# Kernel tuning notes

Measured on AMD Instinct MI355X. Metric: run time of the kernel, lower is better.

## Reference

```python
import jax, jax.numpy as jnp
import numpy as np

B = 16
H_DIM = 512
N_HEADS = 8
HEAD_DIM = H_DIM // N_HEADS  # 64
EPS = 1e-5
DST_LENS = 256 + 16 * np.arange(B)  # ragged dst sizes, total 6016
SRC_LENS = 512 - 8 * np.arange(B)   # ragged src sizes, total 7232


def _pad_info(lens):
    # gather/scatter indices to move between flat ragged layout and [B, Lmax, D]
    lens = np.asarray(lens)
    off = np.concatenate([[0], np.cumsum(lens)[:-1]])
    gid = np.repeat(np.arange(len(lens)), lens)
    pos = np.arange(int(lens.sum())) - np.repeat(off, lens)
    Lmax = int(lens.max())
    mask = jnp.asarray(np.arange(Lmax)[None, :] < lens[:, None])
    return gid, pos, Lmax, mask


def _bn(x, g, b):
    # BatchNorm1d forward with batch statistics (training-mode normalization)
    m = x.mean(0)
    v = ((x - m) ** 2).mean(0)
    return (x - m) / jnp.sqrt(v + EPS) * g + b


def setup_inputs() -> dict:
    key = jax.random.key(0)
    ks = jax.random.split(key, 20)
    total_src = int(SRC_LENS.sum())
    total_dst = int(DST_LENS.sum())
    w = lambda k, shape: jax.random.normal(k, shape, jnp.float32) * 0.02
    return {
        "src_h": jax.random.normal(ks[0], (total_src, H_DIM), jnp.float32),
        "dst_h": jax.random.normal(ks[1], (total_dst, H_DIM), jnp.float32),
        "src_num_verts": jnp.asarray(SRC_LENS, jnp.int32),
        "dst_num_verts": jnp.asarray(DST_LENS, jnp.int32),
        "Wq": w(ks[2], (H_DIM, H_DIM)), "bq": w(ks[3], (H_DIM,)),
        "Wk": w(ks[4], (H_DIM, H_DIM)), "bk": w(ks[5], (H_DIM,)),
        "Wv": w(ks[6], (H_DIM, H_DIM)), "bv": w(ks[7], (H_DIM,)),
        "Wm": w(ks[8], (H_DIM, H_DIM)), "bm": w(ks[9], (H_DIM,)),
        "W1": w(ks[10], (H_DIM, 2 * H_DIM)), "b1": w(ks[11], (H_DIM,)),
        "g1": jnp.ones((H_DIM,), jnp.float32), "be1": jnp.zeros((H_DIM,), jnp.float32),
        "W2": w(ks[12], (H_DIM, H_DIM)), "b2": w(ks[13], (H_DIM,)),
        "g2": jnp.ones((H_DIM,), jnp.float32), "be2": jnp.zeros((H_DIM,), jnp.float32),
    }


def reference(src_h, dst_h, src_num_verts, dst_num_verts,
              Wq, bq, Wk, bk, Wv, bv, Wm, bm,
              W1, b1, g1, be1, W2, b2, g2, be2):
    s_lens = np.asarray(src_num_verts)
    d_lens = np.asarray(dst_num_verts)
    sg, sp, Ls, smask = _pad_info(s_lens)
    dg, dp, Ld, dmask = _pad_info(d_lens)

    # ragged -> padded [B, L, D]
    src_pad = jnp.zeros((B, Ls, H_DIM), src_h.dtype).at[sg, sp].set(src_h)
    dst_pad = jnp.zeros((B, Ld, H_DIM), dst_h.dtype).at[dg, dp].set(dst_h)

    # Conv1d(k=1) projections; channel c = d*num_heads + h -> reshape (head_dim, n_heads)
    q = (dst_pad @ Wq.T + bq).reshape(B, Ld, HEAD_DIM, N_HEADS)
    k = (src_pad @ Wk.T + bk).reshape(B, Ls, HEAD_DIM, N_HEADS)
    v = (src_pad @ Wv.T + bv).reshape(B, Ls, HEAD_DIM, N_HEADS)

    scores = jnp.einsum('bndh,bmdh->bhnm', q, k) / 8.0  # sqrt(head_dim)=8
    scores = jnp.where(smask[:, None, None, :], scores, -1e9)
    attn = jax.nn.softmax(scores, axis=-1)
    o = jnp.einsum('bhnm,bmdh->bndh', attn, v).reshape(B, Ld, H_DIM)
    o = o @ Wm.T + bm  # merge Conv1d(k=1)

    # padded -> ragged
    h_msg = o[dg, dp]  # [total_dst, h_dim]

    h = dst_h
    x = jnp.concatenate([h, h_msg], axis=-1)
    x = _bn(x @ W1.T + b1, g1, be1)
    x = jax.nn.relu(x)
    x = _bn(x @ W2.T + b2, g2, be2)
    return h + x
```

## Files before the change

### kernel.cpp

```cpp
#include <hip/hip_runtime.h>
#include <hip/hip_bf16.h>

#define H_DIM 512
#define N_HEADS 8
#define HEAD_DIM 64
#define NBATCH 16

typedef __attribute__((ext_vector_type(8))) short short8;
typedef __attribute__((ext_vector_type(4))) float floatx4;

typedef unsigned short us16;

#define SW3(r) ((((r) >> 1) & 3) | (((r) & 1) << 2))

#define PERMC(c) ((((c) & 7) << 6) | ((c) >> 3))
#define IPERMC(cp) ((((cp) & 63) << 3) | ((cp) >> 6))

__device__ inline unsigned short f2bf(float f) {
  unsigned int u = __float_as_uint(f);
  unsigned int r = (u + 0x7fffu + ((u >> 16) & 1u)) >> 16;
  return (unsigned short)r;
}

__device__ inline void gld16(const us16* g, us16* l) {
  __builtin_amdgcn_global_load_lds(
      (const __attribute__((address_space(1))) void*)g,
      (__attribute__((address_space(3))) void*)l, 16, 0, 0);
}

__global__ __launch_bounds__(256) void prep_all(
    const float* __restrict__ src_h, const float* __restrict__ dst_h,
    const float* __restrict__ Wq, const float* __restrict__ Wk,
    const float* __restrict__ Wv, const float* __restrict__ W1,
    const float* __restrict__ W2, const float* __restrict__ Wm,
    const float* __restrict__ b1, const float* __restrict__ bm,
    us16* __restrict__ src_bf, us16* __restrict__ dst_bf,
    us16* __restrict__ Wqb, us16* __restrict__ Wkv, us16* __restrict__ Wf,
    us16* __restrict__ W2b, float* __restrict__ b1p, float* __restrict__ st,
    int n_src, int n_dst) {
  __shared__ __align__(16) us16 As[64 * 48];
  __shared__ __align__(16) us16 Bs[64 * 48];
  const int blk = blockIdx.x;
  const int t = threadIdx.x;

  if (blk < 2048) {
    if (blk == 0) {
      float4 z = make_float4(0.f, 0.f, 0.f, 0.f);
      ((float4*)st)[t] = z;
      ((float4*)st)[t + 256] = z;
    }
    const float* srcs[7] = {src_h, dst_h, Wq, Wk, Wv, W1, W2};
    us16* dsts[7] = {src_bf, dst_bf, Wqb, Wkv, Wkv + 262144, Wf, W2b};
    int ns[7] = {n_src, n_dst, 262144, 262144, 262144, 262144, 262144};
    const int md_[7] = {0, 0, 2, 2, 0, 1, 0};
    for (int rg = 0; rg < 7; ++rg) {
      const float* sp = srcs[rg];
      us16* dp = dsts[rg];
      const int mode = md_[rg];
      for (int i = (blk * 256 + t) * 4; i < ns[rg]; i += 2048 * 256 * 4) {
        int js, jd;
        if (mode == 1) {
          js = ((i >> 9) * 1024) + (i & 511);
          jd = js;
        } else if (mode == 2) {
          int r = i >> 9;
          js = i;
          jd = (PERMC(r) << 9) + (i & 511);
        } else {
          js = i; jd = i;
        }
        float4 v = *(const float4*)(sp + js);
        ushort4 o;
        o.x = f2bf(v.x); o.y = f2bf(v.y); o.z = f2bf(v.z); o.w = f2bf(v.w);
        *(ushort4*)(dp + jd) = o;
      }
    }
  } else if (blk < 2112) {
    const int bx = (blk - 2048) & 7, byk = (blk - 2048) >> 3;
    const int w = t >> 6, lane = t & 63;
    const int lane15 = lane & 15, quad = lane >> 4;
    const int wm = w >> 1, wn = w & 1;
    const int bn_ = bx * 64, bk = byk * 64;
    floatx4 acc[2][2];
#pragma unroll
    for (int a = 0; a < 2; ++a)
#pragma unroll
      for (int c = 0; c < 2; ++c) acc[a][c] = (floatx4){0.f, 0.f, 0.f, 0.f};
    for (int j0 = 0; j0 < 512; j0 += 32) {
      {
        int n = t >> 2, jj0 = (t & 3) * 8;
        const float* rp = W1 + (size_t)(bn_ + n) * 1024 + 512 + j0 + jj0;
        float4 va = *(const float4*)(rp);
        float4 vb = *(const float4*)(rp + 4);
        ushort4 pa, pb;
        pa.x = f2bf(va.x); pa.y = f2bf(va.y); pa.z = f2bf(va.z); pa.w = f2bf(va.w);
        pb.x = f2bf(vb.x); pb.y = f2bf(vb.y); pb.z = f2bf(vb.z); pb.w = f2bf(vb.w);
        *(ushort4*)(As + n * 48 + jj0) = pa;
        *(ushort4*)(As + n * 48 + jj0 + 4) = pb;
      }
      {
        int jj = t >> 3, kc0 = (t & 7) * 8;
        const float* rp = Wm + (size_t)(j0 + jj) * 512 + bk + kc0;
        float4 va = *(const float4*)(rp);
        float4 vb = *(const float4*)(rp + 4);
        float vv[8] = {va.x, va.y, va.z, va.w, vb.x, vb.y, vb.z, vb.w};
#pragma unroll
        for (int e = 0; e < 8; ++e) Bs[(kc0 + e) * 48 + jj] = f2bf(vv[e]);
      }
      __syncthreads();
      short8 a_[2], b_[2];
#pragma unroll
      for (int mt = 0; mt < 2; ++mt)
        a_[mt] = *(const short8*)(As + (wm * 32 + mt * 16 + lane15) * 48 + quad * 8);
#pragma unroll
      for (int nt = 0; nt < 2; ++nt)
        b_[nt] = *(const short8*)(Bs + (wn * 32 + nt * 16 + lane15) * 48 + quad * 8);
#pragma unroll
      for (int mt = 0; mt < 2; ++mt)
#pragma unroll
        for (int nt = 0; nt < 2; ++nt)
          acc[mt][nt] = __builtin_amdgcn_mfma_f32_16x16x32_bf16(
              a_[mt], b_[nt], acc[mt][nt], 0, 0, 0);
      __syncthreads();
    }
#pragma unroll
    for (int mt = 0; mt < 2; ++mt) {
      int n0 = bn_ + wm * 32 + mt * 16 + quad * 4;
#pragma unroll
      for (int nt = 0; nt < 2; ++nt) {
        int k = bk + wn * 32 + nt * 16 + lane15;
        int kp = PERMC(k);
#pragma unroll
        for (int r = 0; r < 4; ++r)
          Wf[(size_t)(n0 + r) * 1024 + 512 + kp] = f2bf(acc[mt][nt][r]);
      }
    }
  } else {
    int n = (blk - 2112) * 256 + t;
    if (n < 512) {
      const float* rp = W1 + (size_t)n * 1024 + 512;
      float s = 0.f;
      for (int j = 0; j < 512; j += 4) {
        float4 a = *(const float4*)(rp + j);
        float4 c = *(const float4*)(bm + j);
        s += a.x * c.x + a.y * c.y + a.z * c.z + a.w * c.w;
      }
      b1p[n] = b1[n] + s;
    }
  }
}

__device__ inline void gemm_body(
    const us16* __restrict__ A1, const us16* __restrict__ A2,
    const us16* __restrict__ W,
    const float* __restrict__ bias0, const float* __restrict__ bias1,
    void* __restrict__ C0, void* __restrict__ C1, float* __restrict__ stats,
    int M, int N, int K, int mode, int bx, int by) {
  __shared__ __align__(16) us16 As[2 * 64 * 64];
  __shared__ __align__(16) us16 Bs[2 * 128 * 64];
  const int t = threadIdx.x, w = t >> 6, lane = t & 63;
  const int lane15 = lane & 15, quad = lane >> 4;
  const int bm = bx * 64, bn = by * 128;
  const int lrow = lane >> 3;
  const int sl = lane & 7;

  floatx4 acc[4][2];
#pragma unroll
  for (int a = 0; a < 4; ++a)
#pragma unroll
    for (int c = 0; c < 2; ++c) acc[a][c] = (floatx4){0.f, 0.f, 0.f, 0.f};

  const int nk = K >> 6;

#define ISSUE(i, b)                                                          \
  {                                                                          \
    int k0 = (i) << 6;                                                       \
    const us16* Ab = (k0 < 512) ? A1 : A2;                                   \
    int ka = k0 & 511;                                                       \
    _Pragma("unroll")                                                        \
    for (int p = 0; p < 2; ++p) {                                            \
      int rbase = p * 32 + w * 8;                                            \
      int row = rbase + lrow;                                                \
      int kg = sl ^ SW3(row);                                                \
      gld16(Ab + (size_t)(bm + row) * 512 + ka + kg * 8,                     \
            As + (b) * 4096 + rbase * 64);                                   \
    }                                                                        \
    _Pragma("unroll")                                                        \
    for (int p = 0; p < 4; ++p) {                                            \
      int rbase = p * 32 + w * 8;                                            \
      int row = rbase + lrow;                                                \
      int kg = sl ^ SW3(row);                                                \
      gld16(W + (size_t)(bn + row) * K + k0 + kg * 8,                        \
            Bs + (b) * 8192 + rbase * 64);                                   \
    }                                                                        \
  }

  ISSUE(0, 0);
  if (nk > 1) ISSUE(1, 1);
  for (int i = 0; i < nk; ++i) {
    const int cur = i & 1;
    if (i + 1 < nk) {
      asm volatile("s_waitcnt vmcnt(6)" ::: "memory");
    } else {
      asm volatile("s_waitcnt vmcnt(0)" ::: "memory");
    }
    __builtin_amdgcn_s_barrier();
    asm volatile("" ::: "memory");
#pragma unroll
    for (int kh = 0; kh < 2; ++kh) {
      const int g = kh * 4 + quad;
      short8 a_[4], b_[2];
#pragma unroll
      for (int mt = 0; mt < 4; ++mt) {
        int r = mt * 16 + lane15;
        a_[mt] = *(const short8*)(As + cur * 4096 + r * 64 + (g ^ SW3(r)) * 8);
      }
#pragma unroll
      for (int nt = 0; nt < 2; ++nt) {
        int c = w * 32 + nt * 16 + lane15;
        b_[nt] = *(const short8*)(Bs + cur * 8192 + c * 64 + (g ^ SW3(c)) * 8);
      }
#pragma unroll
      for (int mt = 0; mt < 4; ++mt)
#pragma unroll
        for (int nt = 0; nt < 2; ++nt)
          acc[mt][nt] = __builtin_amdgcn_mfma_f32_16x16x32_bf16(
              a_[mt], b_[nt], acc[mt][nt], 0, 0, 0);
    }
    asm volatile("" ::: "memory");
    __builtin_amdgcn_s_barrier();
    asm volatile("" ::: "memory");
    if (i + 2 < nk) ISSUE(i + 2, cur);
  }
#undef ISSUE

  if (mode == 0) {
#pragma unroll
    for (int nt = 0; nt < 2; ++nt) {
      int col = bn + w * 32 + nt * 16 + lane15;
      float bv = bias0[col];
      float s = 0.f, qq = 0.f;
#pragma unroll
      for (int mt = 0; mt < 4; ++mt) {
        int row0 = bm + mt * 16 + quad * 4;
#pragma unroll
        for (int r = 0; r < 4; ++r) {
          float val = acc[mt][nt][r] + bv;
          ((float*)C0)[(size_t)(row0 + r) * N + col] = val;
          s += val; qq = fmaf(val, val, qq);
        }
      }
      s += __shfl_xor(s, 16); s += __shfl_xor(s, 32);
      qq += __shfl_xor(qq, 16); qq += __shfl_xor(qq, 32);
      if (quad == 0) {
        atomicAdd(&stats[col], s);
        atomicAdd(&stats[512 + col], qq);
      }
    }
  } else if (mode == 1) {
#pragma unroll
    for (int nt = 0; nt < 2; ++nt) {
      int col = bn + w * 32 + nt * 16 + lane15;
      float bv = bias0[IPERMC(col)];
#pragma unroll
      for (int mt = 0; mt < 4; ++mt) {
        int row0 = bm + mt * 16 + quad * 4;
#pragma unroll
        for (int r = 0; r < 4; ++r)
          ((us16*)C0)[(size_t)(row0 + r) * 512 + col] = f2bf(acc[mt][nt][r] + bv);
      }
    }
  } else {
#pragma unroll
    for (int nt = 0; nt < 2; ++nt) {
      int col = bn + w * 32 + nt * 16 + lane15;
      if (col < 512) {
        float bv = bias0[IPERMC(col)];
#pragma unroll
        for (int mt = 0; mt < 4; ++mt) {
          int row0 = bm + mt * 16 + quad * 4;
#pragma unroll
          for (int r = 0; r < 4; ++r)
            ((us16*)C0)[(size_t)(row0 + r) * 512 + col] = f2bf(acc[mt][nt][r] + bv);
        }
      } else {
        int cv = col - 512;
        float bv = bias1[cv];
        int plane = (cv & 7) * 64 + (cv >> 3);
#pragma unroll
        for (int mt = 0; mt < 4; ++mt) {
          int row0 = bm + mt * 16 + quad * 4;
          ushort4 pk;
          pk.x = f2bf(acc[mt][nt][0] + bv);
          pk.y = f2bf(acc[mt][nt][1] + bv);
          pk.z = f2bf(acc[mt][nt][2] + bv);
          pk.w = f2bf(acc[mt][nt][3] + bv);
          *(ushort4*)((us16*)C1 + (size_t)plane * M + row0) = pk;
        }
      }
    }
  }
}

__global__ __launch_bounds__(256) void gemm_ffn(
    const us16* __restrict__ A1, const us16* __restrict__ A2,
    const us16* __restrict__ W,
    const float* __restrict__ bias0, void* __restrict__ C0,
    float* __restrict__ stats, int M, int K) {
  int b = blockIdx.x;
  int i = (b & 7) * ((int)gridDim.x >> 3) + (b >> 3);
  gemm_body(A1, A2, W, bias0, nullptr, C0, nullptr, stats, M, 512, K, 0,
            i >> 2, i & 3);
}

__global__ __launch_bounds__(256) void gemm_qkv(
    const us16* __restrict__ dst_bf, const us16* __restrict__ src_bf,
    const us16* __restrict__ Wqb, const us16* __restrict__ Wkv,
    const float* __restrict__ bq, const float* __restrict__ bk,
    const float* __restrict__ bv,
    us16* __restrict__ Qh, us16* __restrict__ Kh, us16* __restrict__ Vt,
    int Md, int Ms) {
  int b = blockIdx.x;
  int i = (b & 7) * ((int)gridDim.x >> 3) + (b >> 3);
  int nq = (Md / 64) * 4;
  if (i < nq) {
    gemm_body(dst_bf, dst_bf, Wqb, bq, nullptr, Qh, nullptr, nullptr,
              Md, 512, 512, 1, i >> 2, i & 3);
  } else {
    int j = i - nq;
    gemm_body(src_bf, src_bf, Wkv, bk, bv, Kh, Vt, nullptr,
              Ms, 1024, 512, 4, j >> 3, j & 7);
  }
}

__global__ __launch_bounds__(256) void gemm_ffn2bn(
    const float* __restrict__ X1, const us16* __restrict__ W,
    const float* __restrict__ st1, const float* __restrict__ g1,
    const float* __restrict__ be1, const float* __restrict__ b2,
    float* __restrict__ X2, float* __restrict__ st2, int M, float invM) {
  __shared__ __align__(16) us16 As[2 * 64 * 64];
  __shared__ __align__(16) us16 Bs[2 * 128 * 64];
  __shared__ float slt[512], tlt[512];
  int b = blockIdx.x;
  int i0 = (b & 7) * ((int)gridDim.x >> 3) + (b >> 3);
  const int bx = i0 >> 2, by = i0 & 3;
  const int t = threadIdx.x, w = t >> 6, lane = t & 63;
  const int lane15 = lane & 15, quad = lane >> 4;
  const int bm = bx * 64, bn = by * 128;
  const int lrow = lane >> 3;
  const int sl = lane & 7;

  for (int c = t; c < 512; c += 256) {
    float mean = st1[c] * invM;
    float var = fmaf(-mean, mean, st1[512 + c] * invM);
    float inv = rsqrtf(var + 1e-5f) * g1[c];
    slt[c] = inv;
    tlt[c] = be1[c] - mean * inv;
  }
  __syncthreads();

  floatx4 acc[4][2];
#pragma unroll
  for (int a = 0; a < 4; ++a)
#pragma unroll
    for (int c = 0; c < 2; ++c) acc[a][c] = (floatx4){0.f, 0.f, 0.f, 0.f};

  const int arow = t >> 2;
  const int ac4 = (t & 3) * 16;
  const int s0 = (t & 3) * 2;

#define ALOAD(dst, ii)                                                       \
  {                                                                          \
    const float* p_ = X1 + (size_t)(bm + arow) * 512 + ((ii) << 6) + ac4;    \
    dst[0] = *(const float4*)(p_);                                           \
    dst[1] = *(const float4*)(p_ + 4);                                       \
    dst[2] = *(const float4*)(p_ + 8);                                       \
    dst[3] = *(const float4*)(p_ + 12);                                      \
  }

#define BISSUE(ii, bb)                                                       \
  {                                                                          \
    int k0 = (ii) << 6;                                                      \
    _Pragma("unroll")                                                        \
    for (int p = 0; p < 4; ++p) {                                            \
      int rbase = p * 32 + w * 8;                                            \
      int row = rbase + lrow;                                                \
      int kg = sl ^ SW3(row);                                                \
      gld16(W + (size_t)(bn + row) * 512 + k0 + kg * 8,                      \
            Bs + (bb) * 8192 + rbase * 64);                                  \
    }                                                                        \
  }

  float4 areg[2][4];
  ALOAD(areg[0], 0);
  BISSUE(0, 0);
  asm volatile("" ::: "memory");
  ALOAD(areg[1], 1);
  BISSUE(1, 1);

#pragma unroll
  for (int i = 0; i < 8; ++i) {
    const int cur = i & 1;
    if (i + 1 < 8) {
      asm volatile("s_waitcnt vmcnt(8)" ::: "memory");
    } else {
      asm volatile("s_waitcnt vmcnt(0)" ::: "memory");
    }
    {
      const int k0 = i << 6;
      __align__(16) us16 vv[16];
#pragma unroll
      for (int q = 0; q < 4; ++q) {
#pragma unroll
        for (int j = 0; j < 4; ++j) {
          int c = k0 + ac4 + q * 4 + j;
          float x = ((const float*)&areg[cur][q])[j];
          float y = fmaxf(fmaf(x, slt[c], tlt[c]), 0.f);
          vv[q * 4 + j] = f2bf(y);
        }
      }
      us16* base = As + cur * 4096 + arow * 64;
      *(short8*)(base + ((s0 ^ SW3(arow)) * 8)) = *(short8*)&vv[0];
      *(short8*)(base + (((s0 + 1) ^ SW3(arow)) * 8)) = *(short8*)&vv[8];
    }
    asm volatile("s_waitcnt lgkmcnt(0)" ::: "memory");
    __builtin_amdgcn_s_barrier();
    asm volatile("" ::: "memory");
#pragma unroll
    for (int kh = 0; kh < 2; ++kh) {
      const int g = kh * 4 + quad;
      short8 a_[4], b_[2];
#pragma unroll
      for (int mt = 0; mt < 4; ++mt) {
        int r = mt * 16 + lane15;
        a_[mt] = *(const short8*)(As + cur * 4096 + r * 64 + (g ^ SW3(r)) * 8);
      }
#pragma unroll
      for (int nt = 0; nt < 2; ++nt) {
        int c = w * 32 + nt * 16 + lane15;
        b_[nt] = *(const short8*)(Bs + cur * 8192 + c * 64 + (g ^ SW3(c)) * 8);
      }
#pragma unroll
      for (int mt = 0; mt < 4; ++mt)
#pragma unroll
        for (int nt = 0; nt < 2; ++nt)
          acc[mt][nt] = __builtin_amdgcn_mfma_f32_16x16x32_bf16(
              a_[mt], b_[nt], acc[mt][nt], 0, 0, 0);
    }
    asm volatile("" ::: "memory");
    __builtin_amdgcn_s_barrier();
    asm volatile("" ::: "memory");
    if (i + 2 < 8) {
      ALOAD(areg[cur], i + 2);
      BISSUE(i + 2, cur);
    }
  }
#undef ALOAD
#undef BISSUE

#pragma unroll
  for (int nt = 0; nt < 2; ++nt) {
    int col = bn + w * 32 + nt * 16 + lane15;
    float bv = b2[col];
    float s = 0.f, qq = 0.f;
#pragma unroll
    for (int mt = 0; mt < 4; ++mt) {
      int row0 = bm + mt * 16 + quad * 4;
#pragma unroll
      for (int r = 0; r < 4; ++r) {
        float val = acc[mt][nt][r] + bv;
        X2[(size_t)(row0 + r) * 512 + col] = val;
        s += val; qq = fmaf(val, val, qq);
      }
    }
    s += __shfl_xor(s, 16); s += __shfl_xor(s, 32);
    qq += __shfl_xor(qq, 16); qq += __shfl_xor(qq, 32);
    if (quad == 0) {
      atomicAdd(&st2[col], s);
      atomicAdd(&st2[512 + col], qq);
    }
  }
}

__global__ __launch_bounds__(256) void attn_v6(
    const us16* __restrict__ Qh, const us16* __restrict__ Kh,
    const us16* __restrict__ Vt, const int* __restrict__ dlens,
    const int* __restrict__ slens, us16* __restrict__ O,
    int Md, int Ms) {
  const int b = blockIdx.x, h = blockIdx.y, tile = blockIdx.z;
  int doff = 0, soff = 0;
  for (int i = 0; i < NBATCH; ++i)
    if (i < b) { doff += dlens[i]; soff += slens[i]; }
  const int dlen = dlens[b], slen = slens[b];
  if (tile * 64 >= dlen) return;

  __shared__ __align__(16) us16 Ks[2 * 64 * 64];
  __shared__ __align__(16) us16 Vts[2 * 64 * 64];
  __shared__ __align__(16) us16 Pw[4][16 * 72];

  const int t = threadIdx.x, wv = t >> 6, lane = t & 63;
  const int lane15 = lane & 15, quad = lane >> 4;
  const int i0w = tile * 64 + wv * 16;
  const bool active = i0w < dlen;

  const us16* Qp = Qh + ((size_t)(doff + (active ? i0w : 0))) * 512 + h * 64;
  const us16* Kp = Kh + ((size_t)soff) * 512 + h * 64;
  const us16* Vtp = Vt + ((size_t)h * 64) * Ms + soff;

  short8 af0 = *(const short8*)(Qp + (size_t)lane15 * 512 + quad * 8);
  short8 af1 = *(const short8*)(Qp + (size_t)lane15 * 512 + 32 + quad * 8);

  floatx4 oa[4];
#pragma unroll
  for (int nt = 0; nt < 4; ++nt) oa[nt] = (floatx4){0.f, 0.f, 0.f, 0.f};
  float m_r[4] = {-3.0e38f, -3.0e38f, -3.0e38f, -3.0e38f};
  float l_r[4] = {0.f, 0.f, 0.f, 0.f};

  const int nc = (slen + 63) >> 6;

#define KVST(c, bu)                                                       \
  {                                                                       \
    int jb = (c) << 6;                                                    \
    _Pragma("unroll")                                                     \
    for (int p = 0; p < 2; ++p) {                                         \
      int row = wv * 16 + p * 8 + (lane >> 3);                            \
      int slt = lane & 7;                                                 \
      int kg = slt ^ SW3(row);                                            \
      gld16(Kp + (size_t)(jb + row) * 512 + kg * 8,                       \
            Ks + (bu) * 4096 + (wv * 16 + p * 8) * 64);                   \
      gld16(Vtp + (size_t)row * Ms + jb + kg * 8,                         \
            Vts + (bu) * 4096 + (wv * 16 + p * 8) * 64);                  \
    }                                                                     \
  }

  KVST(0, 0);
  if (nc > 1) KVST(1, 1);
  for (int c = 0; c < nc; ++c) {
    const int cur = c & 1;
    if (c + 1 < nc) {
      asm volatile("s_waitcnt vmcnt(4)" ::: "memory");
    } else {
      asm volatile("s_waitcnt vmcnt(0)" ::: "memory");
    }
    __builtin_amdgcn_s_barrier();
    asm volatile("" ::: "memory");

    if (active) {
      const int j0 = c << 6;
      floatx4 s[4];
#pragma unroll
      for (int jt = 0; jt < 4; ++jt) {
        int j = jt * 16 + lane15;
        short8 b0 = *(const short8*)(Ks + cur * 4096 + j * 64 + ((quad ^ SW3(j)) * 8));
        short8 b1 = *(const short8*)(Ks + cur * 4096 + j * 64 + (((4 + quad) ^ SW3(j)) * 8));
        floatx4 a = (floatx4){0.f, 0.f, 0.f, 0.f};
        a = __builtin_amdgcn_mfma_f32_16x16x32_bf16(af0, b0, a, 0, 0, 0);
        a = __builtin_amdgcn_mfma_f32_16x16x32_bf16(af1, b1, a, 0, 0, 0);
        s[jt] = a;
      }
      float mx[4] = {-3.0e38f, -3.0e38f, -3.0e38f, -3.0e38f};
#pragma unroll
      for (int jt = 0; jt < 4; ++jt) {
        bool valid = (j0 + jt * 16 + lane15) < slen;
#pragma unroll
        for (int r = 0; r < 4; ++r) {
          float v = valid ? s[jt][r] * 0.125f : -3.0e38f;
          s[jt][r] = v;
          mx[r] = fmaxf(mx[r], v);
        }
      }
#pragma unroll
      for (int r = 0; r < 4; ++r) {
        mx[r] = fmaxf(mx[r], __shfl_xor(mx[r], 1));
        mx[r] = fmaxf(mx[r], __shfl_xor(mx[r], 2));
        mx[r] = fmaxf(mx[r], __shfl_xor(mx[r], 4));
        mx[r] = fmaxf(mx[r], __shfl_xor(mx[r], 8));
      }
      float al[4], sum[4];
#pragma unroll
      for (int r = 0; r < 4; ++r) {
        float mn = fmaxf(m_r[r], mx[r]);
        al[r] = __expf(m_r[r] - mn);
        m_r[r] = mn;
        sum[r] = 0.f;
      }
#pragma unroll
      for (int jt = 0; jt < 4; ++jt)
#pragma unroll
        for (int r = 0; r < 4; ++r) {
          float e = __expf(s[jt][r] - m_r[r]);
          sum[r] += e;
          Pw[wv][(quad * 4 + r) * 72 + jt * 16 + lane15] = f2bf(e);
        }
#pragma unroll
      for (int r = 0; r < 4; ++r) {
        sum[r] += __shfl_xor(sum[r], 1);
        sum[r] += __shfl_xor(sum[r], 2);
        sum[r] += __shfl_xor(sum[r], 4);
        sum[r] += __shfl_xor(sum[r], 8);
        l_r[r] = l_r[r] * al[r] + sum[r];
      }
#pragma unroll
      for (int nt = 0; nt < 4; ++nt)
#pragma unroll
        for (int r = 0; r < 4; ++r) oa[nt][r] *= al[r];
      short8 pa0 = *(const short8*)(&Pw[wv][lane15 * 72 + quad * 8]);
      short8 pa1 = *(const short8*)(&Pw[wv][lane15 * 72 + 32 + quad * 8]);
#pragma unroll
      for (int nt = 0; nt < 4; ++nt) {
        int d = nt * 16 + lane15;
        short8 v0 = *(const short8*)(Vts + cur * 4096 + d * 64 + ((quad ^ SW3(d)) * 8));
        short8 v1 = *(const short8*)(Vts + cur * 4096 + d * 64 + (((4 + quad) ^ SW3(d)) * 8));
        oa[nt] = __builtin_amdgcn_mfma_f32_16x16x32_bf16(pa0, v0, oa[nt], 0, 0, 0);
        oa[nt] = __builtin_amdgcn_mfma_f32_16x16x32_bf16(pa1, v1, oa[nt], 0, 0, 0);
      }
    }

    asm volatile("" ::: "memory");
    __builtin_amdgcn_s_barrier();
    asm volatile("" ::: "memory");
    if (c + 2 < nc) KVST(c + 2, cur);
  }
#undef KVST

  if (active) {
    float linv[4];
#pragma unroll
    for (int r = 0; r < 4; ++r) linv[r] = 1.f / l_r[r];
#pragma unroll
    for (int r = 0; r < 4; ++r) {
      int i = quad * 4 + r;
      us16* orow = O + (size_t)(doff + i0w + i) * H_DIM + h * 64;
#pragma unroll
      for (int nt = 0; nt < 4; ++nt) {
        int d = nt * 16 + lane15;
        orow[d] = f2bf(oa[nt][r] * linv[r]);
      }
    }
  }
}

__global__ __launch_bounds__(256) void bn2_apply(
    const float* __restrict__ X, const float* __restrict__ stats,
    const float* __restrict__ g, const float* __restrict__ be,
    const float* __restrict__ resid, float* __restrict__ Y,
    int M, float invM) {
  const size_t total4 = (size_t)M * (H_DIM / 4);
  for (size_t i = (size_t)blockIdx.x * 256 + threadIdx.x; i < total4;
       i += (size_t)gridDim.x * 256) {
    int c = (int)((i * 4) & (H_DIM - 1));
    float4 x = ((const float4*)X)[i];
    float4 rr = ((const float4*)resid)[i];
    float4 o;
#pragma unroll
    for (int j = 0; j < 4; ++j) {
      int cc = c + j;
      float mean = stats[cc] * invM;
      float var = fmaf(-mean, mean, stats[H_DIM + cc] * invM);
      float inv = rsqrtf(var + 1e-5f) * g[cc];
      float xv = ((const float*)&x)[j];
      ((float*)&o)[j] = (xv - mean) * inv + be[cc] + ((const float*)&rr)[j];
    }
    ((float4*)Y)[i] = o;
  }
}

extern "C" void kernel_launch(void* const* d_in, const int* in_sizes, int n_in,
                              void* d_out, int out_size, void* d_ws, size_t ws_size,
                              hipStream_t stream) {
  const float* src_h = (const float*)d_in[0];
  const float* dst_h = (const float*)d_in[1];
  const int* s_lens  = (const int*)d_in[2];
  const int* d_lens  = (const int*)d_in[3];
  const float* Wq = (const float*)d_in[4];  const float* bq = (const float*)d_in[5];
  const float* Wk = (const float*)d_in[6];  const float* bk = (const float*)d_in[7];
  const float* Wv = (const float*)d_in[8];  const float* bv = (const float*)d_in[9];
  const float* Wm = (const float*)d_in[10]; const float* bm = (const float*)d_in[11];
  const float* W1 = (const float*)d_in[12]; const float* b1 = (const float*)d_in[13];
  const float* g1 = (const float*)d_in[14]; const float* be1 = (const float*)d_in[15];
  const float* W2 = (const float*)d_in[16]; const float* b2 = (const float*)d_in[17];
  const float* g2 = (const float*)d_in[18]; const float* be2 = (const float*)d_in[19];

  const int total_src = in_sizes[0] / H_DIM;
  const int total_dst = in_sizes[1] / H_DIM;

  char* ws = (char*)d_ws;
  us16* src_bf = (us16*)(ws + 0);
  us16* dst_bf = (us16*)(ws + 7405568);
  us16* wbf    = (us16*)(ws + 13565952);
  float* b1p   = (float*)(ws + 16711680);
  us16* Qh     = (us16*)(ws + 17235968);
  us16* Kh     = (us16*)(ws + 23396352);
  us16* Vt     = (us16*)(ws + 30801920);
  us16* Ob     = (us16*)(ws + 38207488);
  float* st    = (float*)(ws + 50528256);
  float* X1    = (float*)(ws + 17235968);
  float* X2    = (float*)(ws + 30801920);
  float* st1 = st, *st2 = st + 1024;

  us16* Wqb = wbf;
  us16* Wkv = wbf + 262144;
  us16* Wf  = wbf + 786432;
  us16* W2b = wbf + 1310720;

  const int mbd = total_dst / 64;
  const int mbs = total_src / 64;
  const dim3 blk256(256);
  const float invM = 1.f / (float)total_dst;

  prep_all<<<dim3(2114), blk256, 0, stream>>>(
      src_h, dst_h, Wq, Wk, Wv, W1, W2, Wm, b1, bm,
      src_bf, dst_bf, Wqb, Wkv, Wf, W2b, b1p, st,
      total_src * H_DIM, total_dst * H_DIM);

  gemm_qkv<<<dim3(mbd * 4 + mbs * 8), blk256, 0, stream>>>(
      dst_bf, src_bf, Wqb, Wkv, bq, bk, bv, Qh, Kh, Vt, total_dst, total_src);

  attn_v6<<<dim3(NBATCH, N_HEADS, 8), blk256, 0, stream>>>(
      Qh, Kh, Vt, d_lens, s_lens, Ob, total_dst, total_src);

  gemm_ffn<<<dim3(mbd * 4), blk256, 0, stream>>>(
      dst_bf, Ob, Wf, b1p, X1, st1, total_dst, 1024);

  gemm_ffn2bn<<<dim3(mbd * 4), blk256, 0, stream>>>(
      X1, W2b, st1, g1, be1, b2, X2, st2, total_dst, invM);

  bn2_apply<<<dim3(512), blk256, 0, stream>>>(
      X2, st2, g2, be2, dst_h, (float*)d_out, total_dst, invM);
}
```

Measured before the change: 220.0 us.

## Fuse fp32-to-bf16 activation conversion into QKV and FFN1 GEMM loaders

Stops pre-converting src_h and dst_h to bf16 in a separate prep pass. The QKV and FFN1 GEMMs now load fp32 activations into registers, convert them, and write swizzled bf16 tiles to LDS, while Ob still streams in through direct global-to-LDS loads. Weight prep (Wf fold, W1/W2 casts, b1p) moves into extra blocks of the QKV launch, and only the Wq/Wk/Wv casts stay in a small prep kernel. This removes a full write and reread of the activations, but the A-operand loads go through registers and VALU conversion, which may hurt the GEMM pipelines. The bn2_apply grid size also changes.

```diff
diff --git a/kernel.cpp b/kernel.cpp
--- a/kernel.cpp
+++ b/kernel.cpp
@@ -28,141 +28,37 @@
       (__attribute__((address_space(3))) void*)l, 16, 0, 0);
 }
 
-__global__ __launch_bounds__(256) void prep_all(
-    const float* __restrict__ src_h, const float* __restrict__ dst_h,
+__global__ __launch_bounds__(256) void prep0(
     const float* __restrict__ Wq, const float* __restrict__ Wk,
-    const float* __restrict__ Wv, const float* __restrict__ W1,
-    const float* __restrict__ W2, const float* __restrict__ Wm,
-    const float* __restrict__ b1, const float* __restrict__ bm,
-    us16* __restrict__ src_bf, us16* __restrict__ dst_bf,
-    us16* __restrict__ Wqb, us16* __restrict__ Wkv, us16* __restrict__ Wf,
-    us16* __restrict__ W2b, float* __restrict__ b1p, float* __restrict__ st,
-    int n_src, int n_dst) {
-  __shared__ __align__(16) us16 As[64 * 48];
-  __shared__ __align__(16) us16 Bs[64 * 48];
-  const int blk = blockIdx.x;
-  const int t = threadIdx.x;
-
-  if (blk < 2048) {
-    if (blk == 0) {
-      float4 z = make_float4(0.f, 0.f, 0.f, 0.f);
-      ((float4*)st)[t] = z;
-      ((float4*)st)[t + 256] = z;
-    }
-    const float* srcs[7] = {src_h, dst_h, Wq, Wk, Wv, W1, W2};
-    us16* dsts[7] = {src_bf, dst_bf, Wqb, Wkv, Wkv + 262144, Wf, W2b};
-    int ns[7] = {n_src, n_dst, 262144, 262144, 262144, 262144, 262144};
-    const int md_[7] = {0, 0, 2, 2, 0, 1, 0};
-    for (int rg = 0; rg < 7; ++rg) {
-      const float* sp = srcs[rg];
-      us16* dp = dsts[rg];
-      const int mode = md_[rg];
-      for (int i = (blk * 256 + t) * 4; i < ns[rg]; i += 2048 * 256 * 4) {
-        int js, jd;
-        if (mode == 1) {
-          js = ((i >> 9) * 1024) + (i & 511);
-          jd = js;
-        } else if (mode == 2) {
-          int r = i >> 9;
-          js = i;
-          jd = (PERMC(r) << 9) + (i & 511);
-        } else {
-          js = i; jd = i;
-        }
-        float4 v = *(const float4*)(sp + js);
-        ushort4 o;
-        o.x = f2bf(v.x); o.y = f2bf(v.y); o.z = f2bf(v.z); o.w = f2bf(v.w);
-        *(ushort4*)(dp + jd) = o;
-      }
-    }
-  } else if (blk < 2112) {
-    const int bx = (blk - 2048) & 7, byk = (blk - 2048) >> 3;
-    const int w = t >> 6, lane = t & 63;
-    const int lane15 = lane & 15, quad = lane >> 4;
-    const int wm = w >> 1, wn = w & 1;
-    const int bn_ = bx * 64, bk = byk * 64;
-    floatx4 acc[2][2];
-#pragma unroll
-    for (int a = 0; a < 2; ++a)
-#pragma unroll
-      for (int c = 0; c < 2; ++c) acc[a][c] = (floatx4){0.f, 0.f, 0.f, 0.f};
-    for (int j0 = 0; j0 < 512; j0 += 32) {
-      {
-        int n = t >> 2, jj0 = (t & 3) * 8;
-        const float* rp = W1 + (size_t)(bn_ + n) * 1024 + 512 + j0 + jj0;
-        float4 va = *(const float4*)(rp);
-        float4 vb = *(const float4*)(rp + 4);
-        ushort4 pa, pb;
-        pa.x = f2bf(va.x); pa.y = f2bf(va.y); pa.z = f2bf(va.z); pa.w = f2bf(va.w);
-        pb.x = f2bf(vb.x); pb.y = f2bf(vb.y); pb.z = f2bf(vb.z); pb.w = f2bf(vb.w);
-        *(ushort4*)(As + n * 48 + jj0) = pa;
-        *(ushort4*)(As + n * 48 + jj0 + 4) = pb;
-      }
-      {
-        int jj = t >> 3, kc0 = (t & 7) * 8;
-        const float* rp = Wm + (size_t)(j0 + jj) * 512 + bk + kc0;
-        float4 va = *(const float4*)(rp);
-        float4 vb = *(const float4*)(rp + 4);
-        float vv[8] = {va.x, va.y, va.z, va.w, vb.x, vb.y, vb.z, vb.w};
-#pragma unroll
-        for (int e = 0; e < 8; ++e) Bs[(kc0 + e) * 48 + jj] = f2bf(vv[e]);
-      }
-      __syncthreads();
-      short8 a_[2], b_[2];
-#pragma unroll
-      for (int mt = 0; mt < 2; ++mt)
-        a_[mt] = *(const short8*)(As + (wm * 32 + mt * 16 + lane15) * 48 + quad * 8);
-#pragma unroll
-      for (int nt = 0; nt < 2; ++nt)
-        b_[nt] = *(const short8*)(Bs + (wn * 32 + nt * 16 + lane15) * 48 + quad * 8);
-#pragma unroll
-      for (int mt = 0; mt < 2; ++mt)
-#pragma unroll
-        for (int nt = 0; nt < 2; ++nt)
-          acc[mt][nt] = __builtin_amdgcn_mfma_f32_16x16x32_bf16(
-              a_[mt], b_[nt], acc[mt][nt], 0, 0, 0);
-      __syncthreads();
-    }
-#pragma unroll
-    for (int mt = 0; mt < 2; ++mt) {
-      int n0 = bn_ + wm * 32 + mt * 16 + quad * 4;
-#pragma unroll
-      for (int nt = 0; nt < 2; ++nt) {
-        int k = bk + wn * 32 + nt * 16 + lane15;
-        int kp = PERMC(k);
-#pragma unroll
-        for (int r = 0; r < 4; ++r)
-          Wf[(size_t)(n0 + r) * 1024 + 512 + kp] = f2bf(acc[mt][nt][r]);
-      }
-    }
-  } else {
-    int n = (blk - 2112) * 256 + t;
-    if (n < 512) {
-      const float* rp = W1 + (size_t)n * 1024 + 512;
-      float s = 0.f;
-      for (int j = 0; j < 512; j += 4) {
-        float4 a = *(const float4*)(rp + j);
-        float4 c = *(const float4*)(bm + j);
-        s += a.x * c.x + a.y * c.y + a.z * c.z + a.w * c.w;
-      }
-      b1p[n] = b1[n] + s;
-    }
-  }
-}
-
-__device__ inline void gemm_body(
-    const us16* __restrict__ A1, const us16* __restrict__ A2,
-    const us16* __restrict__ W,
+    const float* __restrict__ Wv,
+    us16* __restrict__ Wqb, us16* __restrict__ Wkv, float* __restrict__ st) {
+  const int blk = blockIdx.x, t = threadIdx.x;
+  if (blk == 0) {
+    float4 z = make_float4(0.f, 0.f, 0.f, 0.f);
+    ((float4*)st)[t] = z;
+    ((float4*)st)[t + 256] = z;
+  }
+  const int rg = blk >> 8;
+  const float* sp = (rg == 0) ? Wq : (rg == 1) ? Wk : Wv;
+  us16* dp = (rg == 0) ? Wqb : (rg == 1) ? Wkv : (Wkv + 262144);
+  const int i = (((blk & 255) << 8) + t) << 2;
+  float4 v = *(const float4*)(sp + i);
+  ushort4 o;
+  o.x = f2bf(v.x); o.y = f2bf(v.y); o.z = f2bf(v.z); o.w = f2bf(v.w);
+  int jd = (rg < 2) ? ((PERMC(i >> 9) << 9) + (i & 511)) : i;
+  *(ushort4*)(dp + jd) = o;
+}
+
+__device__ inline void qkv_body(
+    const float* __restrict__ actF, const us16* __restrict__ W,
     const float* __restrict__ bias0, const float* __restrict__ bias1,
-    void* __restrict__ C0, void* __restrict__ C1, float* __restrict__ stats,
-    int M, int N, int K, int mode, int bx, int by) {
-  __shared__ __align__(16) us16 As[2 * 64 * 64];
-  __shared__ __align__(16) us16 Bs[2 * 128 * 64];
+    void* __restrict__ C0, void* __restrict__ C1,
+    int M, int mode, int bx, int by, us16* As, us16* Bs) {
   const int t = threadIdx.x, w = t >> 6, lane = t & 63;
   const int lane15 = lane & 15, quad = lane >> 4;
   const int bm = bx * 64, bn = by * 128;
-  const int lrow = lane >> 3;
-  const int sl = lane & 7;
+  const int lrow = lane >> 3, sl = lane & 7;
+  const int arow = t >> 2, ac4 = (t & 3) * 16, s0 = (t & 3) * 2;
 
   floatx4 acc[4][2];
 #pragma unroll
@@ -170,40 +66,54 @@
 #pragma unroll
     for (int c = 0; c < 2; ++c) acc[a][c] = (floatx4){0.f, 0.f, 0.f, 0.f};
 
-  const int nk = K >> 6;
-
-#define ISSUE(i, b)                                                          \
+#define QALOAD(dst, ii)                                                      \
   {                                                                          \
-    int k0 = (i) << 6;                                                       \
-    const us16* Ab = (k0 < 512) ? A1 : A2;                                   \
-    int ka = k0 & 511;                                                       \
-    _Pragma("unroll")                                                        \
-    for (int p = 0; p < 2; ++p) {                                            \
-      int rbase = p * 32 + w * 8;                                            \
-      int row = rbase + lrow;                                                \
-      int kg = sl ^ SW3(row);                                                \
-      gld16(Ab + (size_t)(bm + row) * 512 + ka + kg * 8,                     \
-            As + (b) * 4096 + rbase * 64);                                   \
-    }                                                                        \
+    const float* p_ = actF + (size_t)(bm + arow) * 512 + ((ii) << 6) + ac4;  \
+    dst[0] = *(const float4*)(p_);                                           \
+    dst[1] = *(const float4*)(p_ + 4);                                       \
+    dst[2] = *(const float4*)(p_ + 8);                                       \
+    dst[3] = *(const float4*)(p_ + 12);                                      \
+  }
+#define QBISS(ii, bb)                                                        \
+  {                                                                          \
+    int k0 = (ii) << 6;                                                      \
     _Pragma("unroll")                                                        \
     for (int p = 0; p < 4; ++p) {                                            \
       int rbase = p * 32 + w * 8;                                            \
       int row = rbase + lrow;                                                \
       int kg = sl ^ SW3(row);                                                \
-      gld16(W + (size_t)(bn + row) * K + k0 + kg * 8,                        \
-            Bs + (b) * 8192 + rbase * 64);                                   \
+      gld16(W + (size_t)(bn + row) * 512 + k0 + kg * 8,                      \
+            Bs + (bb) * 8192 + rbase * 64);                                  \
     }                                                                        \
   }
 
-  ISSUE(0, 0);
-  if (nk > 1) ISSUE(1, 1);
-  for (int i = 0; i < nk; ++i) {
+  float4 areg[2][4];
+  QALOAD(areg[0], 0);
+  QBISS(0, 0);
+  asm volatile("" ::: "memory");
+  QALOAD(areg[1], 1);
+  QBISS(1, 1);
+
+#pragma unroll
+  for (int i = 0; i < 8; ++i) {
     const int cur = i & 1;
-    if (i + 1 < nk) {
-      asm volatile("s_waitcnt vmcnt(6)" ::: "memory");
+    if (i < 7) {
+      asm volatile("s_waitcnt vmcnt(8)" ::: "memory");
     } else {
       asm volatile("s_waitcnt vmcnt(0)" ::: "memory");
     }
+    {
+      __align__(16) us16 vv[16];
+#pragma unroll
+      for (int q = 0; q < 4; ++q)
+#pragma unroll
+        for (int j = 0; j < 4; ++j)
+          vv[q * 4 + j] = f2bf(((const float*)&areg[cur][q])[j]);
+      us16* base = As + cur * 4096 + arow * 64;
+      *(short8*)(base + ((s0 ^ SW3(arow)) * 8)) = *(short8*)&vv[0];
+      *(short8*)(base + (((s0 + 1) ^ SW3(arow)) * 8)) = *(short8*)&vv[8];
+    }
+    asm volatile("s_waitcnt lgkmcnt(0)" ::: "memory");
     __builtin_amdgcn_s_barrier();
     asm volatile("" ::: "memory");
 #pragma unroll
@@ -230,34 +140,15 @@
     asm volatile("" ::: "memory");
     __builtin_amdgcn_s_barrier();
     asm volatile("" ::: "memory");
-    if (i + 2 < nk) ISSUE(i + 2, cur);
-  }
-#undef ISSUE
-
-  if (mode == 0) {
-#pragma unroll
-    for (int nt = 0; nt < 2; ++nt) {
-      int col = bn + w * 32 + nt * 16 + lane15;
-      float bv = bias0[col];
-      float s = 0.f, qq = 0.f;
-#pragma unroll
-      for (int mt = 0; mt < 4; ++mt) {
-        int row0 = bm + mt * 16 + quad * 4;
-#pragma unroll
-        for (int r = 0; r < 4; ++r) {
-          float val = acc[mt][nt][r] + bv;
-          ((float*)C0)[(size_t)(row0 + r) * N + col] = val;
-          s += val; qq = fmaf(val, val, qq);
-        }
-      }
-      s += __shfl_xor(s, 16); s += __shfl_xor(s, 32);
-      qq += __shfl_xor(qq, 16); qq += __shfl_xor(qq, 32);
-      if (quad == 0) {
-        atomicAdd(&stats[col], s);
-        atomicAdd(&stats[512 + col], qq);
-      }
-    }
-  } else if (mode == 1) {
+    if (i + 2 < 8) {
+      QALOAD(areg[cur], i + 2);
+      QBISS(i + 2, cur);
+    }
+  }
+#undef QALOAD
+#undef QBISS
+
+  if (mode == 1) {
 #pragma unroll
     for (int nt = 0; nt < 2; ++nt) {
       int col = bn + w * 32 + nt * 16 + lane15;
@@ -302,34 +193,277 @@
   }
 }
 
-__global__ __launch_bounds__(256) void gemm_ffn(
-    const us16* __restrict__ A1, const us16* __restrict__ A2,
-    const us16* __restrict__ W,
-    const float* __restrict__ bias0, void* __restrict__ C0,
-    float* __restrict__ stats, int M, int K) {
-  int b = blockIdx.x;
-  int i = (b & 7) * ((int)gridDim.x >> 3) + (b >> 3);
-  gemm_body(A1, A2, W, bias0, nullptr, C0, nullptr, stats, M, 512, K, 0,
-            i >> 2, i & 3);
-}
-
 __global__ __launch_bounds__(256) void gemm_qkv(
-    const us16* __restrict__ dst_bf, const us16* __restrict__ src_bf,
+    const float* __restrict__ dstF, const float* __restrict__ srcF,
     const us16* __restrict__ Wqb, const us16* __restrict__ Wkv,
     const float* __restrict__ bq, const float* __restrict__ bk,
     const float* __restrict__ bv,
     us16* __restrict__ Qh, us16* __restrict__ Kh, us16* __restrict__ Vt,
+    const float* __restrict__ W1, const float* __restrict__ Wm,
+    const float* __restrict__ W2, const float* __restrict__ b1,
+    const float* __restrict__ bm,
+    us16* __restrict__ Wf, us16* __restrict__ W2b, float* __restrict__ b1p,
     int Md, int Ms) {
-  int b = blockIdx.x;
-  int i = (b & 7) * ((int)gridDim.x >> 3) + (b >> 3);
-  int nq = (Md / 64) * 4;
+  __shared__ __align__(16) us16 As[2 * 64 * 64];
+  __shared__ __align__(16) us16 Bs[2 * 128 * 64];
+  const int nq = (Md / 64) * 4;
+  const int ngemm = nq + (Ms / 64) * 8;
+  const int blk = blockIdx.x, t = threadIdx.x;
+
+  if (blk >= ngemm) {
+    const int r = blk - ngemm;
+    if (r < 64) {
+      us16* Asw = As;
+      us16* Bsw = As + 3072;
+      const int bx = r & 7, byk = r >> 3;
+      const int w = t >> 6, lane = t & 63;
+      const int lane15 = lane & 15, quad = lane >> 4;
+      const int wm = w >> 1, wn = w & 1;
+      const int bn_ = bx * 64, bk = byk * 64;
+      floatx4 acc[2][2];
+#pragma unroll
+      for (int a = 0; a < 2; ++a)
+#pragma unroll
+        for (int c = 0; c < 2; ++c) acc[a][c] = (floatx4){0.f, 0.f, 0.f, 0.f};
+      for (int j0 = 0; j0 < 512; j0 += 32) {
+        {
+          int n = t >> 2, jj0 = (t & 3) * 8;
+          const float* rp = W1 + (size_t)(bn_ + n) * 1024 + 512 + j0 + jj0;
+          float4 va = *(const float4*)(rp);
+          float4 vb = *(const float4*)(rp + 4);
+          ushort4 pa, pb;
+          pa.x = f2bf(va.x); pa.y = f2bf(va.y); pa.z = f2bf(va.z); pa.w = f2bf(va.w);
+          pb.x = f2bf(vb.x); pb.y = f2bf(vb.y); pb.z = f2bf(vb.z); pb.w = f2bf(vb.w);
+          *(ushort4*)(Asw + n * 48 + jj0) = pa;
+          *(ushort4*)(Asw + n * 48 + jj0 + 4) = pb;
+        }
+        {
+          int jj = t >> 3, kc0 = (t & 7) * 8;
+          const float* rp = Wm + (size_t)(j0 + jj) * 512 + bk + kc0;
+          float4 va = *(const float4*)(rp);
+          float4 vb = *(const float4*)(rp + 4);
+          float vv[8] = {va.x, va.y, va.z, va.w, vb.x, vb.y, vb.z, vb.w};
+#pragma unroll
+          for (int e = 0; e < 8; ++e) Bsw[(kc0 + e) * 48 + jj] = f2bf(vv[e]);
+        }
+        __syncthreads();
+        short8 a_[2], b_[2];
+#pragma unroll
+        for (int mt = 0; mt < 2; ++mt)
+          a_[mt] = *(const short8*)(Asw + (wm * 32 + mt * 16 + lane15) * 48 + quad * 8);
+#pragma unroll
+        for (int nt = 0; nt < 2; ++nt)
+          b_[nt] = *(const short8*)(Bsw + (wn * 32 + nt * 16 + lane15) * 48 + quad * 8);
+#pragma unroll
+        for (int mt = 0; mt < 2; ++mt)
+#pragma unroll
+          for (int nt = 0; nt < 2; ++nt)
+            acc[mt][nt] = __builtin_amdgcn_mfma_f32_16x16x32_bf16(
+                a_[mt], b_[nt], acc[mt][nt], 0, 0, 0);
+        __syncthreads();
+      }
+#pragma unroll
+      for (int mt = 0; mt < 2; ++mt) {
+        int n0 = bn_ + wm * 32 + mt * 16 + quad * 4;
+#pragma unroll
+        for (int nt = 0; nt < 2; ++nt) {
+          int k = bk + wn * 32 + nt * 16 + lane15;
+          int kp = PERMC(k);
+#pragma unroll
+          for (int rr = 0; rr < 4; ++rr)
+            Wf[(size_t)(n0 + rr) * 1024 + 512 + kp] = f2bf(acc[mt][nt][rr]);
+        }
+      }
+    } else if (r < 128) {
+      int idx = r - 64;
+#pragma unroll
+      for (int e = 0; e < 4; ++e) {
+        int i = idx * 4096 + (e * 256 + t) * 4;
+        int j = ((i >> 9) * 1024) + (i & 511);
+        float4 v = *(const float4*)(W1 + j);
+        ushort4 o;
+        o.x = f2bf(v.x); o.y = f2bf(v.y); o.z = f2bf(v.z); o.w = f2bf(v.w);
+        *(ushort4*)(Wf + j) = o;
+      }
+    } else if (r < 192) {
+      int idx = r - 128;
+#pragma unroll
+      for (int e = 0; e < 4; ++e) {
+        int i = idx * 4096 + (e * 256 + t) * 4;
+        float4 v = *(const float4*)(W2 + i);
+        ushort4 o;
+        o.x = f2bf(v.x); o.y = f2bf(v.y); o.z = f2bf(v.z); o.w = f2bf(v.w);
+        *(ushort4*)(W2b + i) = o;
+      }
+    } else if (r < 194) {
+      int n = (r - 192) * 256 + t;
+      if (n < 512) {
+        const float* rp = W1 + (size_t)n * 1024 + 512;
+        float s = 0.f;
+        for (int j = 0; j < 512; j += 4) {
+          float4 a = *(const float4*)(rp + j);
+          float4 c = *(const float4*)(bm + j);
+          s += a.x * c.x + a.y * c.y + a.z * c.z + a.w * c.w;
+        }
+        b1p[n] = b1[n] + s;
+      }
+    }
+    return;
+  }
+
+  int i = (blk & 7) * (ngemm >> 3) + (blk >> 3);
   if (i < nq) {
-    gemm_body(dst_bf, dst_bf, Wqb, bq, nullptr, Qh, nullptr, nullptr,
-              Md, 512, 512, 1, i >> 2, i & 3);
+    qkv_body(dstF, Wqb, bq, nullptr, Qh, nullptr, Md, 1, i >> 2, i & 3, As, Bs);
   } else {
     int j = i - nq;
-    gemm_body(src_bf, src_bf, Wkv, bk, bv, Kh, Vt, nullptr,
-              Ms, 1024, 512, 4, j >> 3, j & 7);
+    qkv_body(srcF, Wkv, bk, bv, Kh, Vt, Ms, 4, j >> 3, j & 7, As, Bs);
+  }
+}
+
+__global__ __launch_bounds__(256) void gemm_ffn1(
+    const float* __restrict__ dstF, const us16* __restrict__ Ob,
+    const us16* __restrict__ Wf, const float* __restrict__ b1p,
+    float* __restrict__ X1, float* __restrict__ st1, int M) {
+  __shared__ __align__(16) us16 As[2 * 64 * 64];
+  __shared__ __align__(16) us16 Bs[2 * 128 * 64];
+  int b = blockIdx.x;
+  int i0 = (b & 7) * ((int)gridDim.x >> 3) + (b >> 3);
+  const int bx = i0 >> 2, by = i0 & 3;
+  const int t = threadIdx.x, w = t >> 6, lane = t & 63;
+  const int lane15 = lane & 15, quad = lane >> 4;
+  const int bm = bx * 64, bn = by * 128;
+  const int lrow = lane >> 3, sl = lane & 7;
+  const int arow = t >> 2, ac4 = (t & 3) * 16, s0 = (t & 3) * 2;
+
+  floatx4 acc[4][2];
+#pragma unroll
+  for (int a = 0; a < 4; ++a)
+#pragma unroll
+    for (int c = 0; c < 2; ++c) acc[a][c] = (floatx4){0.f, 0.f, 0.f, 0.f};
+
+#define F1ALOAD(dst, ii)                                                     \
+  {                                                                          \
+    const float* p_ = dstF + (size_t)(bm + arow) * 512 + ((ii) << 6) + ac4;  \
+    dst[0] = *(const float4*)(p_);                                           \
+    dst[1] = *(const float4*)(p_ + 4);                                       \
+    dst[2] = *(const float4*)(p_ + 8);                                       \
+    dst[3] = *(const float4*)(p_ + 12);                                      \
+  }
+#define F1AGLD(ii, bb)                                                       \
+  {                                                                          \
+    int ka = ((ii) << 6) - 512;                                              \
+    _Pragma("unroll")                                                        \
+    for (int p = 0; p < 2; ++p) {                                            \
+      int rbase = p * 32 + w * 8;                                            \
+      int row = rbase + lrow;                                                \
+      int kg = sl ^ SW3(row);                                                \
+      gld16(Ob + (size_t)(bm + row) * 512 + ka + kg * 8,                     \
+            As + (bb) * 4096 + rbase * 64);                                  \
+    }                                                                        \
+  }
+#define F1BISS(ii, bb)                                                       \
+  {                                                                          \
+    int k0 = (ii) << 6;                                                      \
+    _Pragma("unroll")                                                        \
+    for (int p = 0; p < 4; ++p) {                                            \
+      int rbase = p * 32 + w * 8;                                            \
+      int row = rbase + lrow;                                                \
+      int kg = sl ^ SW3(row);                                                \
+      gld16(Wf + (size_t)(bn + row) * 1024 + k0 + kg * 8,                    \
+            Bs + (bb) * 8192 + rbase * 64);                                  \
+    }                                                                        \
+  }
+
+  float4 areg[2][4];
+  F1ALOAD(areg[0], 0);
+  F1BISS(0, 0);
+  asm volatile("" ::: "memory");
+  F1ALOAD(areg[1], 1);
+  F1BISS(1, 1);
+
+#pragma unroll
+  for (int i = 0; i < 16; ++i) {
+    const int cur = i & 1;
+    if (i == 15) {
+      asm volatile("s_waitcnt vmcnt(0)" ::: "memory");
+    } else if (i < 7) {
+      asm volatile("s_waitcnt vmcnt(8)" ::: "memory");
+    } else {
+      asm volatile("s_waitcnt vmcnt(6)" ::: "memory");
+    }
+    if (i < 8) {
+      __align__(16) us16 vv[16];
+#pragma unroll
+      for (int q = 0; q < 4; ++q)
+#pragma unroll
+        for (int j = 0; j < 4; ++j)
+          vv[q * 4 + j] = f2bf(((const float*)&areg[cur][q])[j]);
+      us16* base = As + cur * 4096 + arow * 64;
+      *(short8*)(base + ((s0 ^ SW3(arow)) * 8)) = *(short8*)&vv[0];
+      *(short8*)(base + (((s0 + 1) ^ SW3(arow)) * 8)) = *(short8*)&vv[8];
+      asm volatile("s_waitcnt lgkmcnt(0)" ::: "memory");
+    }
+    __builtin_amdgcn_s_barrier();
+    asm volatile("" ::: "memory");
+#pragma unroll
+    for (int kh = 0; kh < 2; ++kh) {
+      const int g = kh * 4 + quad;
+      short8 a_[4], b_[2];
+#pragma unroll
+      for (int mt = 0; mt < 4; ++mt) {
+        int r = mt * 16 + lane15;
+        a_[mt] = *(const short8*)(As + cur * 4096 + r * 64 + (g ^ SW3(r)) * 8);
+      }
+#pragma unroll
+      for (int nt = 0; nt < 2; ++nt) {
+        int c = w * 32 + nt * 16 + lane15;
+        b_[nt] = *(const short8*)(Bs + cur * 8192 + c * 64 + (g ^ SW3(c)) * 8);
+      }
+#pragma unroll
+      for (int mt = 0; mt < 4; ++mt)
+#pragma unroll
+        for (int nt = 0; nt < 2; ++nt)
+          acc[mt][nt] = __builtin_amdgcn_mfma_f32_16x16x32_bf16(
+              a_[mt], b_[nt], acc[mt][nt], 0, 0, 0);
+    }
+    asm volatile("" ::: "memory");
+    __builtin_amdgcn_s_barrier();
+    asm volatile("" ::: "memory");
+    if (i + 2 < 16) {
+      if (i + 2 < 8) {
+        F1ALOAD(areg[cur], i + 2);
+        F1BISS(i + 2, cur);
+      } else {
+        F1AGLD(i + 2, cur);
+        F1BISS(i + 2, cur);
+      }
+    }
+  }
+#undef F1ALOAD
+#undef F1AGLD
+#undef F1BISS
+
+#pragma unroll
+  for (int nt = 0; nt < 2; ++nt) {
+    int col = bn + w * 32 + nt * 16 + lane15;
+    float bv = b1p[col];
+    float s = 0.f, qq = 0.f;
+#pragma unroll
+    for (int mt = 0; mt < 4; ++mt) {
+      int row0 = bm + mt * 16 + quad * 4;
+#pragma unroll
+      for (int r = 0; r < 4; ++r) {
+        float val = acc[mt][nt][r] + bv;
+        X1[(size_t)(row0 + r) * 512 + col] = val;
+        s += val; qq = fmaf(val, val, qq);
+      }
+    }
+    s += __shfl_xor(s, 16); s += __shfl_xor(s, 32);
+    qq += __shfl_xor(qq, 16); qq += __shfl_xor(qq, 32);
+    if (quad == 0) {
+      atomicAdd(&st1[col], s);
+      atomicAdd(&st1[512 + col], qq);
+    }
   }
 }
 
@@ -347,8 +481,8 @@
   const int t = threadIdx.x, w = t >> 6, lane = t & 63;
   const int lane15 = lane & 15, quad = lane >> 4;
   const int bm = bx * 64, bn = by * 128;
-  const int lrow = lane >> 3;
-  const int sl = lane & 7;
+  const int lrow = lane >> 3, sl = lane & 7;
+  const int arow = t >> 2, ac4 = (t & 3) * 16, s0 = (t & 3) * 2;
 
   for (int c = t; c < 512; c += 256) {
     float mean = st1[c] * invM;
@@ -364,10 +498,6 @@
   for (int a = 0; a < 4; ++a)
 #pragma unroll
     for (int c = 0; c < 2; ++c) acc[a][c] = (floatx4){0.f, 0.f, 0.f, 0.f};
-
-  const int arow = t >> 2;
-  const int ac4 = (t & 3) * 16;
-  const int s0 = (t & 3) * 2;
 
 #define ALOAD(dst, ii)                                                       \
   {                                                                          \
@@ -377,7 +507,6 @@
     dst[2] = *(const float4*)(p_ + 8);                                       \
     dst[3] = *(const float4*)(p_ + 12);                                      \
   }
-
 #define BISSUE(ii, bb)                                                       \
   {                                                                          \
     int k0 = (ii) << 6;                                                      \
@@ -685,17 +814,15 @@
   const int total_dst = in_sizes[1] / H_DIM;
 
   char* ws = (char*)d_ws;
-  us16* src_bf = (us16*)(ws + 0);
-  us16* dst_bf = (us16*)(ws + 7405568);
-  us16* wbf    = (us16*)(ws + 13565952);
-  float* b1p   = (float*)(ws + 16711680);
-  us16* Qh     = (us16*)(ws + 17235968);
-  us16* Kh     = (us16*)(ws + 23396352);
-  us16* Vt     = (us16*)(ws + 30801920);
-  us16* Ob     = (us16*)(ws + 38207488);
-  float* st    = (float*)(ws + 50528256);
-  float* X1    = (float*)(ws + 17235968);
-  float* X2    = (float*)(ws + 30801920);
+  us16* wbf  = (us16*)(ws + 0);
+  float* b1p = (float*)(ws + 3145728);
+  float* st  = (float*)(ws + 3147776);
+  us16* Qh   = (us16*)(ws + 3155968);
+  us16* Kh   = (us16*)(ws + 9316352);
+  us16* Vt   = (us16*)(ws + 16721920);
+  us16* Ob   = (us16*)(ws + 24127488);
+  float* X1  = (float*)(ws + 3155968);
+  float* X2  = (float*)(ws + 16721920);
   float* st1 = st, *st2 = st + 1024;
 
   us16* Wqb = wbf;
@@ -705,26 +832,25 @@
 
   const int mbd = total_dst / 64;
   const int mbs = total_src / 64;
+  const int ngemm = mbd * 4 + mbs * 8;
   const dim3 blk256(256);
   const float invM = 1.f / (float)total_dst;
 
-  prep_all<<<dim3(2114), blk256, 0, stream>>>(
-      src_h, dst_h, Wq, Wk, Wv, W1, W2, Wm, b1, bm,
-      src_bf, dst_bf, Wqb, Wkv, Wf, W2b, b1p, st,
-      total_src * H_DIM, total_dst * H_DIM);
-
-  gemm_qkv<<<dim3(mbd * 4 + mbs * 8), blk256, 0, stream>>>(
-      dst_bf, src_bf, Wqb, Wkv, bq, bk, bv, Qh, Kh, Vt, total_dst, total_src);
+  prep0<<<dim3(768), blk256, 0, stream>>>(Wq, Wk, Wv, Wqb, Wkv, st);
+
+  gemm_qkv<<<dim3(ngemm + 194), blk256, 0, stream>>>(
+      dst_h, src_h, Wqb, Wkv, bq, bk, bv, Qh, Kh, Vt,
+      W1, Wm, W2, b1, bm, Wf, W2b, b1p, total_dst, total_src);
 
   attn_v6<<<dim3(NBATCH, N_HEADS, 8), blk256, 0, stream>>>(
       Qh, Kh, Vt, d_lens, s_lens, Ob, total_dst, total_src);
 
-  gemm_ffn<<<dim3(mbd * 4), blk256, 0, stream>>>(
-      dst_bf, Ob, Wf, b1p, X1, st1, total_dst, 1024);
+  gemm_ffn1<<<dim3(mbd * 4), blk256, 0, stream>>>(
+      dst_h, Ob, Wf, b1p, X1, st1, total_dst);
 
   gemm_ffn2bn<<<dim3(mbd * 4), blk256, 0, stream>>>(
       X1, W2b, st1, g1, be1, b2, X2, st2, total_dst, invM);
 
-  bn2_apply<<<dim3(512), blk256, 0, stream>>>(
+  bn2_apply<<<dim3(2048), blk256, 0, stream>>>(
       X2, st2, g2, be2, dst_h, (float*)d_out, total_dst, invM);
 }
```

After: 220.4 us. No clear change (+0.2%).
